# Kernel optimization log

Measured on AMD Instinct MI355X. Metric: run time of the kernel, lower is better.

## Reference

```python
import jax, jax.numpy as jnp
import numpy as np

EPS = 1e-10
BETA = 1.0
N_TH = 21
N, C = 131072, 1000


def _entropy(p):
    # -sum(p * log(clamp(p, eps)), axis=1)  (clamp is min-only, as in torch)
    return -jnp.sum(p * jnp.log(jnp.clip(p, EPS)), axis=1)


def setup_inputs() -> dict:
    key = jax.random.key(0)
    k1, k2 = jax.random.split(key)
    logits = jax.random.normal(k1, (N, C), dtype=jnp.float32)
    probs = jax.nn.softmax(logits, axis=1)  # valid row-wise probabilities
    lab = jax.random.randint(k2, (N,), 0, C)
    y = jax.nn.one_hot(lab, C, dtype=jnp.float32)
    return {"probs": probs, "y": y}


def reference(probs, y):
    confidences = jnp.max(probs, axis=1)          # [N]
    predictions = jnp.argmax(probs, axis=1)       # [N]
    # Faithful to source: argmax over the FLATTENED y -> scalar, broadcast below.
    label = jnp.argmax(y)
    unc = _entropy(probs)                         # [N] predictive uncertainty (type=0)

    th = jnp.linspace(0.0, 1.0, N_TH, dtype=probs.dtype)   # [21]
    umin, umax = jnp.min(unc), jnp.max(unc)
    unc_th = umin + th * (umax - umin)            # [21]

    acc = (label == predictions)                  # [N], scalar-vs-vector compare (as in source)
    t = jnp.tanh(unc)                             # [N]

    # Per-sample weights for the four AvU counters (mask via where == boolean indexing)
    w_ac = jnp.where(acc, confidences * (1.0 - t), 0.0)
    w_au = jnp.where(acc, confidences * t, 0.0)
    w_ic = jnp.where(~acc, (1.0 - confidences) * (1.0 - t), 0.0)
    w_iu = jnp.where(~acc, (1.0 - confidences) * t, 0.0)

    # Vectorize the 21-threshold loop: [21, N] indicator, matvec reductions.
    le = (unc[None, :] <= unc_th[:, None]).astype(probs.dtype)  # [21, N]
    gt = 1.0 - le
    n_ac = le @ w_ac                               # [21]
    n_ic = le @ w_ic
    n_au = gt @ w_au
    n_iu = gt @ w_iu

    avu = (n_ac + n_iu) / (n_ac + n_au + n_ic + n_iu + EPS)    # [21]

    # trapz over increasing th (direction = +1)
    dx = jnp.diff(th)
    auc_avu = jnp.sum((avu[1:] + avu[:-1]) * 0.5 * dx)

    ce = jnp.mean(-jnp.sum(y * jnp.log(jnp.clip(probs, EPS)), axis=1))
    avu_loss = -BETA * jnp.log(auc_avu + EPS) + ce
    return (avu_loss, ce)
```

## Files before the change

kernel.cpp:

```cpp
#include <hip/hip_runtime.h>
#include <hip/hip_bf16.h>

#define EPSF 1e-10f
#define CDIM 1000

struct Scalars {
  double ce_tot;
  float umin, umax;
  unsigned label;
  unsigned pad;
  float hist[4][22];
};

__device__ __forceinline__ void argmax_combine(float& v, unsigned& i, float ov, unsigned oi) {
  if (ov > v || (ov == v && oi < i)) { v = ov; i = oi; }
}

__global__ __launch_bounds__(256)
void k_rowstats(const float* __restrict__ probs, const float* __restrict__ y,
                int n, float* __restrict__ conf, float* __restrict__ uncA,
                unsigned* __restrict__ pred,
                double* __restrict__ blk_ce, unsigned long long* __restrict__ blk_key,
                float* __restrict__ blk_umin, float* __restrict__ blk_umax)
{
  const int lane = threadIdx.x & 63;
  const int wid  = threadIdx.x >> 6;
  const int row  = blockIdx.x * 4 + wid;

  __shared__ double s_ce[4];
  __shared__ unsigned long long s_key[4];
  __shared__ float s_umin[4], s_umax[4];
  __shared__ int s_valid[4];

  if (row < n) {
    const float4* p4 = reinterpret_cast<const float4*>(probs + (size_t)row * CDIM);
    const float4* y4 = reinterpret_cast<const float4*>(y + (size_t)row * CDIM);
    float acc_pl = 0.f, acc_yl = 0.f;
    float bv = -1.f;      unsigned bi = 0;
    float ybv = -1.f;     unsigned ybi = 0;
    for (int c = lane; c < CDIM / 4; c += 64) {
      float4 p = p4[c];
      float4 q = y4[c];
      const float pe[4] = {p.x, p.y, p.z, p.w};
      const float qe[4] = {q.x, q.y, q.z, q.w};
#pragma unroll
      for (int e = 0; e < 4; ++e) {
        float pv = pe[e], yv = qe[e];
        float lp = __logf(fmaxf(pv, EPSF));
        acc_pl = fmaf(pv, lp, acc_pl);
        acc_yl = fmaf(yv, lp, acc_yl);
        unsigned j = 4u * (unsigned)c + (unsigned)e;
        if (pv > bv)  { bv = pv;   bi = j; }
        if (yv > ybv) { ybv = yv;  ybi = j; }
      }
    }
    for (int m = 32; m > 0; m >>= 1) {
      acc_pl += __shfl_xor(acc_pl, m, 64);
      acc_yl += __shfl_xor(acc_yl, m, 64);
      float ov = __shfl_xor(bv, m, 64);  unsigned oi = __shfl_xor(bi, m, 64);
      argmax_combine(bv, bi, ov, oi);
      float oyv = __shfl_xor(ybv, m, 64); unsigned oyi = __shfl_xor(ybi, m, 64);
      argmax_combine(ybv, ybi, oyv, oyi);
    }
    if (lane == 0) {
      float u = -acc_pl;
      conf[row] = bv;
      pred[row] = bi;
      uncA[row] = u;
      s_ce[wid]  = (double)acc_yl;
      s_key[wid] = ((unsigned long long)(~__float_as_uint(ybv)) << 32)
                 | (unsigned long long)((unsigned)row * (unsigned)CDIM + ybi);
      s_umin[wid] = u; s_umax[wid] = u;
      s_valid[wid] = 1;
    }
  } else if (lane == 0) {
    s_valid[wid] = 0;
  }
  __syncthreads();
  if (threadIdx.x == 0) {
    double ce = 0.0;
    unsigned long long key = ~0ull;
    float mn = 3.4e38f, mx = -3.4e38f;
#pragma unroll
    for (int w = 0; w < 4; ++w) {
      if (s_valid[w]) {
        ce += s_ce[w];
        if (s_key[w] < key) key = s_key[w];
        mn = fminf(mn, s_umin[w]);
        mx = fmaxf(mx, s_umax[w]);
      }
    }
    blk_ce[blockIdx.x]  = ce;
    blk_key[blockIdx.x] = key;
    blk_umin[blockIdx.x] = mn;
    blk_umax[blockIdx.x] = mx;
  }
}

__global__ __launch_bounds__(1024)
void k_reduce(const double* __restrict__ blk_ce, const unsigned long long* __restrict__ blk_key,
              const float* __restrict__ blk_umin, const float* __restrict__ blk_umax,
              int nb, Scalars* sc)
{
  __shared__ double sd[1024];
  __shared__ unsigned long long sk[1024];
  __shared__ float smn[1024], smx[1024];
  int t = threadIdx.x;
  double ce = 0.0; unsigned long long key = ~0ull;
  float mn = 3.4e38f, mx = -3.4e38f;
  for (int i = t; i < nb; i += 1024) {
    ce += blk_ce[i];
    unsigned long long k = blk_key[i];
    if (k < key) key = k;
    mn = fminf(mn, blk_umin[i]);
    mx = fmaxf(mx, blk_umax[i]);
  }
  sd[t] = ce; sk[t] = key; smn[t] = mn; smx[t] = mx;
  __syncthreads();
  for (int s = 512; s > 0; s >>= 1) {
    if (t < s) {
      sd[t] += sd[t + s];
      if (sk[t + s] < sk[t]) sk[t] = sk[t + s];
      smn[t] = fminf(smn[t], smn[t + s]);
      smx[t] = fmaxf(smx[t], smx[t + s]);
    }
    __syncthreads();
  }
  if (t == 0) {
    sc->ce_tot = sd[0];
    sc->umin = smn[0];
    sc->umax = smx[0];
    sc->label = (unsigned)(sk[0] & 0xFFFFFFFFull);
  }
  if (t < 88) ((float*)sc->hist)[t] = 0.f;
}

__global__ __launch_bounds__(256)
void k_counters(const float* __restrict__ conf, const float* __restrict__ uncA,
                const unsigned* __restrict__ pred, Scalars* __restrict__ sc, int n)
{
  __shared__ float lh[88];
  for (int i = threadIdx.x; i < 88; i += 256) lh[i] = 0.f;
  __syncthreads();
  const float umin = sc->umin, umax = sc->umax;
  const unsigned label = sc->label;
  const float range = umax - umin;
  for (int i = blockIdx.x * 256 + threadIdx.x; i < n; i += gridDim.x * 256) {
    float c = conf[i], u = uncA[i];
    unsigned p = pred[i];
    float t = tanhf(u);
    int k0 = 21;
#pragma unroll
    for (int k = 0; k < 21; ++k) {
      float thv = umin + ((float)k / 20.0f) * range;
      if (u <= thv) { k0 = k; break; }
    }
    bool acc = (p == label);
    float w1 = acc ? c * (1.f - t) : (1.f - c) * (1.f - t);
    float w2 = acc ? c * t        : (1.f - c) * t;
    int b = acc ? 0 : 2;
    atomicAdd(&lh[b * 22 + k0], w1);
    atomicAdd(&lh[(b + 1) * 22 + k0], w2);
  }
  __syncthreads();
  float* gh = (float*)sc->hist;
  for (int i = threadIdx.x; i < 88; i += 256) {
    if (lh[i] != 0.f) atomicAdd(&gh[i], lh[i]);
  }
}

__global__ void k_final(const Scalars* __restrict__ sc, float* __restrict__ out, int n)
{
  if (threadIdx.x != 0 || blockIdx.x != 0) return;
  const float* hAC = sc->hist[0];
  const float* hAU = sc->hist[1];
  const float* hIC = sc->hist[2];
  const float* hIU = sc->hist[3];
  float totAU = 0.f, totIU = 0.f;
  for (int j = 0; j < 22; ++j) { totAU += hAU[j]; totIU += hIU[j]; }
  float sAC = 0.f, sIC = 0.f, cAU = 0.f, cIU = 0.f;
  float auc = 0.f, prev_avu = 0.f, prev_th = 0.f;
  for (int k = 0; k < 21; ++k) {
    sAC += hAC[k]; sIC += hIC[k]; cAU += hAU[k]; cIU += hIU[k];
    float nac = sAC, nic = sIC;
    float nau = totAU - cAU, niu = totIU - cIU;
    float avu = (nac + niu) / (nac + nau + nic + niu + EPSF);
    float th = (float)k / 20.0f;
    if (k > 0) auc += (avu + prev_avu) * 0.5f * (th - prev_th);
    prev_avu = avu; prev_th = th;
  }
  float ce = (float)(-sc->ce_tot / (double)n);
  float avu_loss = -1.0f * logf(auc + EPSF) + ce;
  out[0] = avu_loss;
  out[1] = ce;
}

extern "C" void kernel_launch(void* const* d_in, const int* in_sizes, int n_in,
                              void* d_out, int out_size, void* d_ws, size_t ws_size,
                              hipStream_t stream) {
  const float* probs = (const float*)d_in[0];
  const float* y     = (const float*)d_in[1];
  const int total = in_sizes[0];
  const int N = total / CDIM;
  const int NB = (N + 3) / 4;

  char* base = (char*)d_ws;
  Scalars* sc = (Scalars*)base;
  double* blk_ce = (double*)(base + 1024);
  unsigned long long* blk_key = (unsigned long long*)(blk_ce + NB);
  float* blk_umin = (float*)(blk_key + NB);
  float* blk_umax = blk_umin + NB;
  float* conf = blk_umax + NB;
  float* uncA = conf + N;
  unsigned* pred = (unsigned*)(uncA + N);

  k_rowstats<<<NB, 256, 0, stream>>>(probs, y, N, conf, uncA, pred,
                                     blk_ce, blk_key, blk_umin, blk_umax);
  k_reduce<<<1, 1024, 0, stream>>>(blk_ce, blk_key, blk_umin, blk_umax, NB, sc);
  k_counters<<<512, 256, 0, stream>>>(conf, uncA, pred, sc, N);
  k_final<<<1, 1, 0, stream>>>(sc, (float*)d_out, N);
}
```

Before: 987.8 us.

## Preload row data into registers, widen blocks, fuse final kernel via ticket

The row-stats kernel now issues all of a wave's vector loads for probs and y up front into register arrays before any compute, so more memory requests are in flight per wave. Blocks grow from 4 to 8 rows (512 threads). The separate single-thread final kernel is removed: the last k_counters block to finish, found with an atomic ticket counter, computes the AUC and loss. This saves one launch, at the cost of more registers per thread and a serialized tail in that last block.

```diff
diff --git a/kernel.cpp b/kernel.cpp
--- a/kernel.cpp
+++ b/kernel.cpp
@@ -3,12 +3,15 @@
 
 #define EPSF 1e-10f
 #define CDIM 1000
+#define ROWS_PER_BLOCK 8
+
+typedef float f32x4 __attribute__((ext_vector_type(4)));
 
 struct Scalars {
   double ce_tot;
   float umin, umax;
   unsigned label;
-  unsigned pad;
+  unsigned ticket;
   float hist[4][22];
 };
 
@@ -16,8 +19,8 @@
   if (ov > v || (ov == v && oi < i)) { v = ov; i = oi; }
 }
 
-__global__ __launch_bounds__(256)
-void k_rowstats(const float* __restrict__ probs, const float* __restrict__ y,
+__global__ __launch_bounds__(512)
+void k_rowstats(const f32x4* __restrict__ probs4, const f32x4* __restrict__ y4,
                 int n, float* __restrict__ conf, float* __restrict__ uncA,
                 unsigned* __restrict__ pred,
                 double* __restrict__ blk_ce, unsigned long long* __restrict__ blk_key,
@@ -25,31 +28,38 @@
 {
   const int lane = threadIdx.x & 63;
   const int wid  = threadIdx.x >> 6;
-  const int row  = blockIdx.x * 4 + wid;
-
-  __shared__ double s_ce[4];
-  __shared__ unsigned long long s_key[4];
-  __shared__ float s_umin[4], s_umax[4];
-  __shared__ int s_valid[4];
+  const int row  = blockIdx.x * ROWS_PER_BLOCK + wid;
+
+  __shared__ double s_ce[ROWS_PER_BLOCK];
+  __shared__ unsigned long long s_key[ROWS_PER_BLOCK];
+  __shared__ float s_umin[ROWS_PER_BLOCK], s_umax[ROWS_PER_BLOCK];
+  __shared__ int s_valid[ROWS_PER_BLOCK];
 
   if (row < n) {
-    const float4* p4 = reinterpret_cast<const float4*>(probs + (size_t)row * CDIM);
-    const float4* y4 = reinterpret_cast<const float4*>(y + (size_t)row * CDIM);
+    const f32x4* p4 = probs4 + (size_t)row * (CDIM / 4);
+    const f32x4* q4 = y4     + (size_t)row * (CDIM / 4);
+
+    f32x4 pr[4], qr[4];
+#pragma unroll
+    for (int it = 0; it < 4; ++it) {
+      const int c = lane + it * 64;
+      if (c < CDIM / 4) { pr[it] = p4[c]; qr[it] = q4[c]; }
+      else              { pr[it] = (f32x4)0.f; qr[it] = (f32x4)0.f; }
+    }
+
     float acc_pl = 0.f, acc_yl = 0.f;
-    float bv = -1.f;      unsigned bi = 0;
-    float ybv = -1.f;     unsigned ybi = 0;
-    for (int c = lane; c < CDIM / 4; c += 64) {
-      float4 p = p4[c];
-      float4 q = y4[c];
-      const float pe[4] = {p.x, p.y, p.z, p.w};
-      const float qe[4] = {q.x, q.y, q.z, q.w};
+    float bv = -1.f;  unsigned bi = 0;
+    float ybv = -1.f; unsigned ybi = 0;
+#pragma unroll
+    for (int it = 0; it < 4; ++it) {
+      const unsigned cbase = 4u * (unsigned)(lane + it * 64);
 #pragma unroll
       for (int e = 0; e < 4; ++e) {
-        float pv = pe[e], yv = qe[e];
+        float pv = pr[it][e], yv = qr[it][e];
         float lp = __logf(fmaxf(pv, EPSF));
         acc_pl = fmaf(pv, lp, acc_pl);
         acc_yl = fmaf(yv, lp, acc_yl);
-        unsigned j = 4u * (unsigned)c + (unsigned)e;
+        unsigned j = cbase + (unsigned)e;
         if (pv > bv)  { bv = pv;   bi = j; }
         if (yv > ybv) { ybv = yv;  ybi = j; }
       }
@@ -82,7 +92,7 @@
     unsigned long long key = ~0ull;
     float mn = 3.4e38f, mx = -3.4e38f;
 #pragma unroll
-    for (int w = 0; w < 4; ++w) {
+    for (int w = 0; w < ROWS_PER_BLOCK; ++w) {
       if (s_valid[w]) {
         ce += s_ce[w];
         if (s_key[w] < key) key = s_key[w];
@@ -131,13 +141,15 @@
     sc->umin = smn[0];
     sc->umax = smx[0];
     sc->label = (unsigned)(sk[0] & 0xFFFFFFFFull);
-  }
-  if (t < 88) ((float*)sc->hist)[t] = 0.f;
+    sc->ticket = 0u;
+  }
+  if (t < 88) (&sc->hist[0][0])[t] = 0.f;
 }
 
 __global__ __launch_bounds__(256)
 void k_counters(const float* __restrict__ conf, const float* __restrict__ uncA,
-                const unsigned* __restrict__ pred, Scalars* __restrict__ sc, int n)
+                const unsigned* __restrict__ pred, Scalars* __restrict__ sc,
+                int n, float* __restrict__ out, int nblocks)
 {
   __shared__ float lh[88];
   for (int i = threadIdx.x; i < 88; i += 256) lh[i] = 0.f;
@@ -163,36 +175,42 @@
     atomicAdd(&lh[(b + 1) * 22 + k0], w2);
   }
   __syncthreads();
-  float* gh = (float*)sc->hist;
+  float* gh = &sc->hist[0][0];
   for (int i = threadIdx.x; i < 88; i += 256) {
     if (lh[i] != 0.f) atomicAdd(&gh[i], lh[i]);
   }
-}
-
-__global__ void k_final(const Scalars* __restrict__ sc, float* __restrict__ out, int n)
-{
-  if (threadIdx.x != 0 || blockIdx.x != 0) return;
-  const float* hAC = sc->hist[0];
-  const float* hAU = sc->hist[1];
-  const float* hIC = sc->hist[2];
-  const float* hIU = sc->hist[3];
-  float totAU = 0.f, totIU = 0.f;
-  for (int j = 0; j < 22; ++j) { totAU += hAU[j]; totIU += hIU[j]; }
-  float sAC = 0.f, sIC = 0.f, cAU = 0.f, cIU = 0.f;
-  float auc = 0.f, prev_avu = 0.f, prev_th = 0.f;
-  for (int k = 0; k < 21; ++k) {
-    sAC += hAC[k]; sIC += hIC[k]; cAU += hAU[k]; cIU += hIU[k];
-    float nac = sAC, nic = sIC;
-    float nau = totAU - cAU, niu = totIU - cIU;
-    float avu = (nac + niu) / (nac + nau + nic + niu + EPSF);
-    float th = (float)k / 20.0f;
-    if (k > 0) auc += (avu + prev_avu) * 0.5f * (th - prev_th);
-    prev_avu = avu; prev_th = th;
-  }
-  float ce = (float)(-sc->ce_tot / (double)n);
-  float avu_loss = -1.0f * logf(auc + EPSF) + ce;
-  out[0] = avu_loss;
-  out[1] = ce;
+  __syncthreads();
+
+  if (threadIdx.x == 0) {
+    __threadfence();
+    unsigned old = atomicAdd(&sc->ticket, 1u);
+    if (old == (unsigned)nblocks - 1) {
+      __threadfence();
+      float h[88];
+      for (int i = 0; i < 88; ++i) h[i] = atomicAdd(&gh[i], 0.f);
+      const float* hAC = h +  0;
+      const float* hAU = h + 22;
+      const float* hIC = h + 44;
+      const float* hIU = h + 66;
+      float totAU = 0.f, totIU = 0.f;
+      for (int j = 0; j < 22; ++j) { totAU += hAU[j]; totIU += hIU[j]; }
+      float sAC = 0.f, sIC = 0.f, cAU = 0.f, cIU = 0.f;
+      float auc = 0.f, prev_avu = 0.f, prev_th = 0.f;
+      for (int k = 0; k < 21; ++k) {
+        sAC += hAC[k]; sIC += hIC[k]; cAU += hAU[k]; cIU += hIU[k];
+        float nac = sAC, nic = sIC;
+        float nau = totAU - cAU, niu = totIU - cIU;
+        float avu = (nac + niu) / (nac + nau + nic + niu + EPSF);
+        float th = (float)k / 20.0f;
+        if (k > 0) auc += (avu + prev_avu) * 0.5f * (th - prev_th);
+        prev_avu = avu; prev_th = th;
+      }
+      float ce = (float)(-sc->ce_tot / (double)n);
+      float avu_loss = -1.0f * logf(auc + EPSF) + ce;
+      out[0] = avu_loss;
+      out[1] = ce;
+    }
+  }
 }
 
 extern "C" void kernel_launch(void* const* d_in, const int* in_sizes, int n_in,
@@ -202,7 +220,7 @@
   const float* y     = (const float*)d_in[1];
   const int total = in_sizes[0];
   const int N = total / CDIM;
-  const int NB = (N + 3) / 4;
+  const int NB = (N + ROWS_PER_BLOCK - 1) / ROWS_PER_BLOCK;
 
   char* base = (char*)d_ws;
   Scalars* sc = (Scalars*)base;
@@ -214,9 +232,11 @@
   float* uncA = conf + N;
   unsigned* pred = (unsigned*)(uncA + N);
 
-  k_rowstats<<<NB, 256, 0, stream>>>(probs, y, N, conf, uncA, pred,
+  const int NCB = 512;
+
+  k_rowstats<<<NB, 512, 0, stream>>>((const f32x4*)probs, (const f32x4*)y, N,
+                                     conf, uncA, pred,
                                      blk_ce, blk_key, blk_umin, blk_umax);
   k_reduce<<<1, 1024, 0, stream>>>(blk_ce, blk_key, blk_umin, blk_umax, NB, sc);
-  k_counters<<<512, 256, 0, stream>>>(conf, uncA, pred, sc, N);
-  k_final<<<1, 1, 0, stream>>>(sc, (float*)d_out, N);
-}
+  k_counters<<<NCB, 256, 0, stream>>>(conf, uncA, pred, sc, N, (float*)d_out, NCB);
+}
```

Result: no change. 1.002 ms (+1.4%).
